# Kernel tuning notes

Measured on AMD Instinct MI355X. Metric: run time of the kernel, lower is better.

The kernel has to match this reference:

```python
import jax, jax.numpy as jnp
import numpy as np

B, S, V = 8, 512, 32000

def setup_inputs() -> dict:
    key = jax.random.key(0)
    k1, k2, k3 = jax.random.split(key, 3)
    predict = jax.random.normal(k1, (B, S, V), dtype=jnp.float32)
    target = jax.random.randint(k2, (B, S), 0, V, dtype=jnp.int64)
    # word lengths in [1, S] so every example has at least one valid token
    mask = jax.random.randint(k3, (B, 1), 1, S + 1, dtype=jnp.int64)
    return {"predict": predict, "target": target, "mask": mask}

def reference(predict, target, mask):
    # predict: [B, S, V], target: [B, S], mask: [B, 1] with mask[:,0] = word_len
    logp = jax.nn.log_softmax(predict, axis=-1)                       # [B, S, V]
    tok_nll = -jnp.take_along_axis(logp, target[..., None], axis=-1)[..., 0]  # [B, S]
    word_len = mask[:, 0]                                             # [B]
    valid = (jnp.arange(predict.shape[1])[None, :] < word_len[:, None])       # [B, S]
    per_example = jnp.sum(tok_nll * valid, axis=1) / word_len.astype(tok_nll.dtype)  # mean over first word_len tokens
    return jnp.mean(per_example)
```

## Files before the change

### kernel.cpp

```cpp
#include <hip/hip_runtime.h>
#include <math.h>

#define BB 8
#define SS 512
#define VV 32000
#define ROWS (BB * SS)
#define CHUNKS 4
#define CF4 2000

typedef float f4 __attribute__((ext_vector_type(4)));

__global__ __launch_bounds__(256) void chunk_sumexp_kernel(
    const float* __restrict__ predict,
    const int*   __restrict__ mask,
    float*       __restrict__ ws)
{
    const int bid   = blockIdx.x;
    const int row   = bid >> 2;
    const int chunk = bid & 3;
    const int b     = row >> 9;
    const int s     = row & 511;
    if (s >= mask[b]) return;

    const f4* rp4 = (const f4*)(predict + (size_t)row * VV) + (size_t)chunk * CF4;
    const int tid = threadIdx.x;

    f4 v0 = __builtin_nontemporal_load(rp4 + tid);
    f4 v1 = __builtin_nontemporal_load(rp4 + tid + 256);
    f4 v2 = __builtin_nontemporal_load(rp4 + tid + 512);
    f4 v3 = __builtin_nontemporal_load(rp4 + tid + 768);
    f4 v4 = __builtin_nontemporal_load(rp4 + tid + 1024);
    f4 v5 = __builtin_nontemporal_load(rp4 + tid + 1280);
    f4 v6 = __builtin_nontemporal_load(rp4 + tid + 1536);
    float s7 = 0.0f;
    if (tid < CF4 - 7 * 256) {
        f4 v7 = __builtin_nontemporal_load(rp4 + tid + 1792);
        s7 = __expf(v7.x) + __expf(v7.y) + __expf(v7.z) + __expf(v7.w);
    }

    float sum = s7
        + __expf(v0.x) + __expf(v0.y) + __expf(v0.z) + __expf(v0.w)
        + __expf(v1.x) + __expf(v1.y) + __expf(v1.z) + __expf(v1.w)
        + __expf(v2.x) + __expf(v2.y) + __expf(v2.z) + __expf(v2.w)
        + __expf(v3.x) + __expf(v3.y) + __expf(v3.z) + __expf(v3.w)
        + __expf(v4.x) + __expf(v4.y) + __expf(v4.z) + __expf(v4.w)
        + __expf(v5.x) + __expf(v5.y) + __expf(v5.z) + __expf(v5.w)
        + __expf(v6.x) + __expf(v6.y) + __expf(v6.z) + __expf(v6.w);

    #pragma unroll
    for (int off = 32; off > 0; off >>= 1)
        sum += __shfl_down(sum, off, 64);

    __shared__ float ssum[4];
    if ((tid & 63) == 0) ssum[tid >> 6] = sum;
    __syncthreads();
    if (tid == 0)
        ws[bid] = ssum[0] + ssum[1] + ssum[2] + ssum[3];
}

__global__ __launch_bounds__(256) void finalize_kernel(
    const float* __restrict__ predict,
    const int*   __restrict__ target,
    const int*   __restrict__ mask,
    const float* __restrict__ ws,
    float*       __restrict__ out)
{
    const int tid = threadIdx.x;

    __shared__ int wls[BB];
    if (tid < BB) wls[tid] = mask[tid];
    __syncthreads();

    float4 w4[ROWS / 256];
    int    tg[ROWS / 256];
    float  xt[ROWS / 256];

    #pragma unroll
    for (int k = 0; k < ROWS / 256; ++k) {
        const int r = tid + k * 256;
        tg[k] = target[r];
        w4[k] = ((const float4*)ws)[r];
    }

    #pragma unroll
    for (int k = 0; k < ROWS / 256; ++k) {
        const int r = tid + k * 256;
        xt[k] = predict[(size_t)r * VV + tg[k]];
    }

    float acc = 0.0f;
    #pragma unroll
    for (int k = 0; k < ROWS / 256; ++k) {
        const int r  = tid + k * 256;
        const int s  = r & 511;
        const int wl = wls[r >> 9];
        if (s < wl) {
            const float4 p = w4[k];
            const float  S = (p.x + p.y) + (p.z + p.w);
            acc += (__logf(S) - xt[k]) / ((float)wl * (float)BB);
        }
    }

    #pragma unroll
    for (int off = 32; off > 0; off >>= 1)
        acc += __shfl_down(acc, off, 64);

    __shared__ float ssum[4];
    if ((tid & 63) == 0) ssum[tid >> 6] = acc;
    __syncthreads();
    if (tid == 0)
        out[0] = ssum[0] + ssum[1] + ssum[2] + ssum[3];
}

extern "C" void kernel_launch(void* const* d_in, const int* in_sizes, int n_in,
                              void* d_out, int out_size, void* d_ws, size_t ws_size,
                              hipStream_t stream) {
    const float* predict = (const float*)d_in[0];
    const int*   target  = (const int*)  d_in[1];
    const int*   mask    = (const int*)  d_in[2];
    float* out = (float*)d_out;
    float* ws  = (float*)d_ws;

    chunk_sumexp_kernel<<<ROWS * CHUNKS, 256, 0, stream>>>(predict, mask, ws);
    finalize_kernel<<<1, 256, 0, stream>>>(predict, target, mask, ws, out);
}
```

Baseline: 597.5 us.

## Use grid-stride persistent blocks and per-wave partial sums for sumexp

The sumexp kernel now launches a fixed grid of 2048 blocks that loop over row-chunk units, instead of one block per unit. Each wavefront writes its own partial sum to the workspace, which removes the shared-memory reduction and __syncthreads from each unit; the finalize kernel then sums 16 partials per row. The mask is loaded into shared memory once per block. The aim is to cut block launch and scheduling overhead and to drop the intra-block sync, at the cost of a static work split that may balance poorly across masked rows and a larger workspace read in finalize.

```diff
diff --git a/kernel.cpp b/kernel.cpp
--- a/kernel.cpp
+++ b/kernel.cpp
@@ -7,6 +7,8 @@
 #define ROWS (BB * SS)
 #define CHUNKS 4
 #define CF4 2000
+#define UNITS (ROWS * CHUNKS)
+#define GRID1 2048
 
 typedef float f4 __attribute__((ext_vector_type(4)));
 
@@ -15,47 +17,50 @@
     const int*   __restrict__ mask,
     float*       __restrict__ ws)
 {
-    const int bid   = blockIdx.x;
-    const int row   = bid >> 2;
-    const int chunk = bid & 3;
-    const int b     = row >> 9;
-    const int s     = row & 511;
-    if (s >= mask[b]) return;
-
-    const f4* rp4 = (const f4*)(predict + (size_t)row * VV) + (size_t)chunk * CF4;
     const int tid = threadIdx.x;
 
-    f4 v0 = __builtin_nontemporal_load(rp4 + tid);
-    f4 v1 = __builtin_nontemporal_load(rp4 + tid + 256);
-    f4 v2 = __builtin_nontemporal_load(rp4 + tid + 512);
-    f4 v3 = __builtin_nontemporal_load(rp4 + tid + 768);
-    f4 v4 = __builtin_nontemporal_load(rp4 + tid + 1024);
-    f4 v5 = __builtin_nontemporal_load(rp4 + tid + 1280);
-    f4 v6 = __builtin_nontemporal_load(rp4 + tid + 1536);
-    float s7 = 0.0f;
-    if (tid < CF4 - 7 * 256) {
-        f4 v7 = __builtin_nontemporal_load(rp4 + tid + 1792);
-        s7 = __expf(v7.x) + __expf(v7.y) + __expf(v7.z) + __expf(v7.w);
+    __shared__ int wls[BB];
+    if (tid < BB) wls[tid] = mask[tid];
+    __syncthreads();
+
+    for (int u = blockIdx.x; u < UNITS; u += GRID1) {
+        const int row = u >> 2;
+        const int b   = row >> 9;
+        const int s   = row & 511;
+        if (s >= wls[b]) continue;
+
+        const int chunk = u & 3;
+        const f4* rp4 = (const f4*)(predict + (size_t)row * VV) + (size_t)chunk * CF4;
+
+        f4 v0 = __builtin_nontemporal_load(rp4 + tid);
+        f4 v1 = __builtin_nontemporal_load(rp4 + tid + 256);
+        f4 v2 = __builtin_nontemporal_load(rp4 + tid + 512);
+        f4 v3 = __builtin_nontemporal_load(rp4 + tid + 768);
+        f4 v4 = __builtin_nontemporal_load(rp4 + tid + 1024);
+        f4 v5 = __builtin_nontemporal_load(rp4 + tid + 1280);
+        f4 v6 = __builtin_nontemporal_load(rp4 + tid + 1536);
+        float s7 = 0.0f;
+        if (tid < CF4 - 7 * 256) {
+            f4 v7 = __builtin_nontemporal_load(rp4 + tid + 1792);
+            s7 = __expf(v7.x) + __expf(v7.y) + __expf(v7.z) + __expf(v7.w);
+        }
+
+        float sum = s7
+            + __expf(v0.x) + __expf(v0.y) + __expf(v0.z) + __expf(v0.w)
+            + __expf(v1.x) + __expf(v1.y) + __expf(v1.z) + __expf(v1.w)
+            + __expf(v2.x) + __expf(v2.y) + __expf(v2.z) + __expf(v2.w)
+            + __expf(v3.x) + __expf(v3.y) + __expf(v3.z) + __expf(v3.w)
+            + __expf(v4.x) + __expf(v4.y) + __expf(v4.z) + __expf(v4.w)
+            + __expf(v5.x) + __expf(v5.y) + __expf(v5.z) + __expf(v5.w)
+            + __expf(v6.x) + __expf(v6.y) + __expf(v6.z) + __expf(v6.w);
+
+        #pragma unroll
+        for (int off = 32; off > 0; off >>= 1)
+            sum += __shfl_down(sum, off, 64);
+
+        if ((tid & 63) == 0)
+            ws[u * 4 + (tid >> 6)] = sum;
     }
-
-    float sum = s7
-        + __expf(v0.x) + __expf(v0.y) + __expf(v0.z) + __expf(v0.w)
-        + __expf(v1.x) + __expf(v1.y) + __expf(v1.z) + __expf(v1.w)
-        + __expf(v2.x) + __expf(v2.y) + __expf(v2.z) + __expf(v2.w)
-        + __expf(v3.x) + __expf(v3.y) + __expf(v3.z) + __expf(v3.w)
-        + __expf(v4.x) + __expf(v4.y) + __expf(v4.z) + __expf(v4.w)
-        + __expf(v5.x) + __expf(v5.y) + __expf(v5.z) + __expf(v5.w)
-        + __expf(v6.x) + __expf(v6.y) + __expf(v6.z) + __expf(v6.w);
-
-    #pragma unroll
-    for (int off = 32; off > 0; off >>= 1)
-        sum += __shfl_down(sum, off, 64);
-
-    __shared__ float ssum[4];
-    if ((tid & 63) == 0) ssum[tid >> 6] = sum;
-    __syncthreads();
-    if (tid == 0)
-        ws[bid] = ssum[0] + ssum[1] + ssum[2] + ssum[3];
 }
 
 __global__ __launch_bounds__(256) void finalize_kernel(
@@ -71,15 +76,14 @@
     if (tid < BB) wls[tid] = mask[tid];
     __syncthreads();
 
-    float4 w4[ROWS / 256];
-    int    tg[ROWS / 256];
-    float  xt[ROWS / 256];
+    int   tg[ROWS / 256];
+    float xt[ROWS / 256];
+    float S [ROWS / 256];
 
     #pragma unroll
     for (int k = 0; k < ROWS / 256; ++k) {
         const int r = tid + k * 256;
         tg[k] = target[r];
-        w4[k] = ((const float4*)ws)[r];
     }
 
     #pragma unroll
@@ -88,17 +92,23 @@
         xt[k] = predict[(size_t)r * VV + tg[k]];
     }
 
+    #pragma unroll
+    for (int k = 0; k < ROWS / 256; ++k) {
+        const int r = tid + k * 256;
+        const float4* wp = (const float4*)ws + r * 4;
+        const float4 a = wp[0], b2 = wp[1], c = wp[2], d = wp[3];
+        S[k] = ((a.x + a.y) + (a.z + a.w)) + ((b2.x + b2.y) + (b2.z + b2.w))
+             + ((c.x + c.y) + (c.z + c.w)) + ((d.x + d.y) + (d.z + d.w));
+    }
+
     float acc = 0.0f;
     #pragma unroll
     for (int k = 0; k < ROWS / 256; ++k) {
         const int r  = tid + k * 256;
         const int s  = r & 511;
         const int wl = wls[r >> 9];
-        if (s < wl) {
-            const float4 p = w4[k];
-            const float  S = (p.x + p.y) + (p.z + p.w);
-            acc += (__logf(S) - xt[k]) / ((float)wl * (float)BB);
-        }
+        if (s < wl)
+            acc += (__logf(S[k]) - xt[k]) / ((float)wl * (float)BB);
     }
 
     #pragma unroll
@@ -121,6 +131,6 @@
     float* out = (float*)d_out;
     float* ws  = (float*)d_ws;
 
-    chunk_sumexp_kernel<<<ROWS * CHUNKS, 256, 0, stream>>>(predict, mask, ws);
+    chunk_sumexp_kernel<<<GRID1, 256, 0, stream>>>(predict, mask, ws);
     finalize_kernel<<<1, 256, 0, stream>>>(predict, target, mask, ws, out);
 }
```

Result: no change. 607.8 us (+1.7%).
